# Kernel optimization log

Hardware: AMD Instinct MI355X
Metric: run time of the kernel (lower is better)

Reference implementation:

```python
import jax, jax.numpy as jnp
import numpy as np

K = 64        # num_clusters
S1 = 5        # num_shadow + 1
C = 128       # dim
ALPHA = 1500.0
EPS = 1e-12


def setup_inputs() -> dict:
    key = jax.random.key(0)
    k1, k2 = jax.random.split(key)
    x = jax.random.normal(k1, (8, C, 44, 44), dtype=jnp.float32)
    centroids = jax.random.normal(k2, (K, S1, C), dtype=jnp.float32) * 0.01
    return {"x": x, "centroids": centroids}


def reference(x, centroids):
    N = x.shape[0]
    # conv params derived from centroids, as in _init_params
    w = (2.0 * ALPHA) * centroids.reshape(K * S1, C)            # (K*S1, C)
    b = -ALPHA * jnp.linalg.norm(centroids.reshape(K * S1, C), axis=1)  # (K*S1,)

    xf = x.reshape(N, C, -1)                                    # (N, C, P)
    # 1x1 conv == GEMM over channel dim
    logits = jnp.einsum('mc,ncp->nmp', w, xf) + b[None, :, None]
    logits = logits.reshape(N, K, S1, -1)                       # (N, K, S1, P)

    soft_alpha = jax.nn.softmax(logits[:, :, 0:1, :], axis=1)   # (N, K, 1, P)
    soft_beta = jax.nn.softmax(logits, axis=2)[:, :, 0:1, :]    # (N, K, 1, P)
    soft_assign = soft_alpha * soft_beta                        # (N, K, 1, P)

    # residual = x - rep_centroid; then residual *= (1 + soft_assign); sum over P.
    # sum_p (x[n,c,p] - rep[k,c]) * w[n,k,p]
    #   = einsum(w, x) - rep[k,c] * sum_p w[n,k,p]   (same math, no (N,K,C,P) tensor)
    w_assign = 1.0 + soft_assign[:, :, 0, :]                    # (N, K, P)
    rep = centroids[:, 0, :]                                    # (K, C)
    out = jnp.einsum('nkp,ncp->nkc', w_assign, xf) \
          - rep[None, :, :] * jnp.sum(w_assign, axis=-1)[:, :, None]  # (N, K, C)

    # intra-cluster L2 normalize (dim=2), flatten, global L2 normalize
    out = out / jnp.maximum(jnp.linalg.norm(out, axis=2, keepdims=True), EPS)
    flat = out.reshape(N, -1)
    flat = flat / jnp.maximum(jnp.linalg.norm(flat, axis=1, keepdims=True), EPS)
    return (flat, soft_assign)
```

## Files before the change

### kernel.cpp

```cpp
#include <hip/hip_runtime.h>
#include <math.h>

#define NB 8
#define KC 64
#define S1C 5
#define CC 128
#define PP 1936
#define MM 320
#define PT 64
#define NPT 31
#define NTILE (NB * NPT)
#define ALPHAF 1500.0f
#define EPSF 1e-12f

#define WS_CENPK 65536
#define WS_GBIAS 512
#define WS_HDR   (WS_CENPK + WS_GBIAS)
#define WS_PART  ((size_t)NTILE * KC * CC)
#define WS_MAIN_FLOATS (WS_HDR + WS_PART + (size_t)NTILE * KC)

typedef __attribute__((ext_vector_type(8))) short short8;
typedef __attribute__((ext_vector_type(4))) float f32x4;

__device__ __forceinline__ unsigned pack_bf16s(float x) {
    unsigned u  = __float_as_uint(x);
    unsigned hi = u & 0xffff0000u;
    float lo    = x - __uint_as_float(hi);
    return hi | (__float_as_uint(lo) >> 16);
}

__device__ __forceinline__ void unpack8(const int4 q0, const int4 q1,
                                        short8& h, short8& l) {
    const int d[8] = {q0.x, q0.y, q0.z, q0.w, q1.x, q1.y, q1.z, q1.w};
#pragma unroll
    for (int j = 0; j < 8; ++j) {
        h[j] = (short)((unsigned)d[j] >> 16);
        l[j] = (short)((unsigned)d[j] & 0xffffu);
    }
}

__device__ __forceinline__ void split8(const float4 a, const float4 b,
                                       short8& h, short8& l) {
    const float f[8] = {a.x, a.y, a.z, a.w, b.x, b.y, b.z, b.w};
#pragma unroll
    for (int j = 0; j < 8; ++j) {
        const unsigned u  = __float_as_uint(f[j]);
        const unsigned hi = u & 0xffff0000u;
        const float lo    = f[j] - __uint_as_float(hi);
        h[j] = (short)(hi >> 16);
        l[j] = (short)(__float_as_uint(lo) >> 16);
    }
}

__global__ __launch_bounds__(64) void k0_pack(
    const float* __restrict__ cen, unsigned* __restrict__ cenPk,
    float* __restrict__ gbias)
{
    const int nt   = blockIdx.x;
    const int l    = threadIdx.x;
    const int l15  = l & 15;
    const int quad = l >> 4;
    const int mp   = nt * 16 + l15;
    const int s    = mp & 7;
    const bool valid = (s < 5);
    const int wrow = 5 * (mp >> 3) + s;
    short8* dst8 = (short8*)cenPk;
    float ss = 0.f;
#pragma unroll
    for (int ks = 0; ks < 4; ++ks) {
        float4 v0 = make_float4(0.f, 0.f, 0.f, 0.f), v1 = v0;
        if (valid) {
            const float* wp = cen + (size_t)wrow * CC + ks * 32 + quad * 8;
            v0 = *(const float4*)wp;
            v1 = *(const float4*)(wp + 4);
        }
        ss += v0.x * v0.x + v0.y * v0.y + v0.z * v0.z + v0.w * v0.w
            + v1.x * v1.x + v1.y * v1.y + v1.z * v1.z + v1.w * v1.w;
        short8 h, lo;
        split8(v0, v1, h, lo);
        const int base = ((ks * 32 + nt) * 64 + l) * 2;
        dst8[base]     = h;
        dst8[base + 1] = lo;
    }
    ss += __shfl_xor(ss, 16);
    ss += __shfl_xor(ss, 32);
    if (quad == 0) gbias[mp] = valid ? (-ALPHAF * sqrtf(ss)) : -3.0e38f;
}

__global__ __launch_bounds__(1024, 4) void k1_main(
    const float* __restrict__ x, const unsigned* __restrict__ cenPk,
    const float* __restrict__ gbias,
    float* __restrict__ sa_out, float* __restrict__ outC,
    float* __restrict__ outS, int mode)
{
    __shared__ unsigned xbuf[CC * 68];
    __shared__ unsigned war[KC * 68];
    __shared__ float2   ap[16 * 66];

    const int tid  = threadIdx.x;
    const int lane = tid & 63;
    const int wid  = tid >> 6;
    const int quad = lane >> 4;
    const int l15  = lane & 15;
    const int bx   = blockIdx.x;
    const int n    = bx / NPT;
    const int pt   = bx - n * NPT;
    const int p0   = pt * PT;

    float4 bvf[2];
#pragma unroll
    for (int i = 0; i < 2; ++i)
        bvf[i] = *(const float4*)(gbias + (2 * wid + i) * 16 + quad * 4);
    const short8* cpk8 = (const short8*)cenPk;
    short8 ch0[2], cl0[2];
#pragma unroll
    for (int i = 0; i < 2; ++i) {
        const int boff = ((2 * wid + i) * 64 + lane) * 2;
        ch0[i] = cpk8[boff];
        cl0[i] = cpk8[boff + 1];
    }

    const float* xn = x + (size_t)n * CC * PP;
    const int sc  = tid >> 3;
    const int spo = (tid & 7) * 8;
    unsigned pk[8];
    {
        float4 v0 = make_float4(0.f, 0.f, 0.f, 0.f), v1 = v0;
        if (p0 + spo < PP) {
            const float* src = xn + (size_t)sc * PP + p0 + spo;
            v0 = *(const float4*)src;
            v1 = *(const float4*)(src + 4);
        }
        pk[0] = pack_bf16s(v0.x); pk[1] = pack_bf16s(v0.y);
        pk[2] = pack_bf16s(v0.z); pk[3] = pack_bf16s(v0.w);
        pk[4] = pack_bf16s(v1.x); pk[5] = pack_bf16s(v1.y);
        pk[6] = pack_bf16s(v1.z); pk[7] = pack_bf16s(v1.w);
#pragma unroll
        for (int j = 0; j < 8; ++j) xbuf[(spo + j) * 132 + sc] = pk[j];
    }
    __syncthreads();

    f32x4 dacc[4][2];
#pragma unroll
    for (int a = 0; a < 4; ++a) {
        dacc[a][0] = (f32x4){0.f, 0.f, 0.f, 0.f};
        dacc[a][1] = (f32x4){0.f, 0.f, 0.f, 0.f};
    }

    auto mfma_step = [&](const int ksoff, const short8 ch[2], const short8 cl[2]) {
#pragma unroll
        for (int a = 0; a < 4; ++a) {
            const int abase = (a * 16 + l15) * 132 + ksoff + quad * 8;
            const int4 q0 = *(const int4*)(&xbuf[abase]);
            const int4 q1 = *(const int4*)(&xbuf[abase + 4]);
            short8 xh, xl;
            unpack8(q0, q1, xh, xl);
#pragma unroll
            for (int i = 0; i < 2; ++i) {
                dacc[a][i] = __builtin_amdgcn_mfma_f32_16x16x32_bf16(ch[i], xh, dacc[a][i], 0, 0, 0);
                dacc[a][i] = __builtin_amdgcn_mfma_f32_16x16x32_bf16(ch[i], xl, dacc[a][i], 0, 0, 0);
                dacc[a][i] = __builtin_amdgcn_mfma_f32_16x16x32_bf16(cl[i], xh, dacc[a][i], 0, 0, 0);
            }
        }
    };

    mfma_step(0, ch0, cl0);
#pragma unroll 1
    for (int ks = 1; ks < 4; ++ks) {
        short8 ch[2], cl[2];
#pragma unroll
        for (int i = 0; i < 2; ++i) {
            const int boff = ((ks * 32 + 2 * wid + i) * 64 + lane) * 2;
            ch[i] = cpk8[boff];
            cl[i] = cpk8[boff + 1];
        }
        mfma_step(ks * 32, ch, cl);
    }

#pragma unroll
    for (int i = 0; i < 2; ++i) {
        const float* bvp = (const float*)&bvf[i];
#pragma unroll
        for (int a = 0; a < 4; ++a)
#pragma unroll
            for (int r = 0; r < 4; ++r)
                dacc[a][i][r] = 2.f * ALPHAF * dacc[a][i][r] + bvp[r];
    }

#pragma unroll
    for (int a = 0; a < 4; ++a) {
        const float l0 = dacc[a][0][0];
        const float l1 = dacc[a][1][0];
        const float m2 = fmaxf(l0, l1);
        const float mo = __shfl_xor(m2, 32);
        const float m4 = fmaxf(m2, mo);
        float se = __expf(l0 - m4) + __expf(l1 - m4);
        se += __shfl_xor(se, 32);
        if ((lane & 48) == 0) ap[wid * 66 + a * 16 + l15] = make_float2(m4, se);
    }
    __syncthreads();

    *(int4*)(&xbuf[sc * 68 + spo])     = *(const int4*)&pk[0];
    *(int4*)(&xbuf[sc * 68 + spo + 4]) = *(const int4*)&pk[4];

    float gmv, arv;
    {
        float gm = -3.0e38f;
#pragma unroll
        for (int w = 0; w < 16; ++w) gm = fmaxf(gm, ap[w * 66 + lane].x);
        float s = 0.f;
#pragma unroll
        for (int w = 0; w < 16; ++w) {
            const float2 v = ap[w * 66 + lane];
            s += v.y * __expf(v.x - gm);
        }
        gmv = gm; arv = 1.0f / s;
    }

    const int  kb  = 4 * wid + ((lane >> 5) & 1);
    const bool evq = ((lane & 16) == 0);
    float psum2[2] = {0.f, 0.f};
#pragma unroll
    for (int a = 0; a < 4; ++a) {
        const int p = a * 16 + l15;
        const float gm_p = __shfl(gmv, p);
        const float ar_p = __shfl(arv, p);
        const bool pvalid = (p0 + p) < PP;
#pragma unroll
        for (int i = 0; i < 2; ++i) {
            const f32x4 lg = dacc[a][i];
            const float s4 = __shfl_xor(lg[0], 16);
            float m5 = fmaxf(fmaxf(lg[0], lg[1]), fmaxf(lg[2], lg[3]));
            m5 = fmaxf(m5, s4);
            const float e0 = __expf(lg[0] - m5);
            const float d5 = e0 + __expf(lg[1] - m5) + __expf(lg[2] - m5)
                           + __expf(lg[3] - m5) + __expf(s4 - m5);
            const float sa = __expf(lg[0] - gm_p) * ar_p * (e0 / d5);
            const float wa = pvalid ? (1.0f + sa) : 0.0f;
            if (evq) war[(kb + 2 * i) * 68 + p] = pack_bf16s(wa);
            psum2[i] += wa;
        }
    }
#pragma unroll
    for (int i = 0; i < 2; ++i) {
        float s = psum2[i];
        s += __shfl_xor(s, 1);
        s += __shfl_xor(s, 2);
        s += __shfl_xor(s, 4);
        s += __shfl_xor(s, 8);
        if ((lane & 31) == 0) {
            const int k = kb + 2 * i;
            if (mode == 0) outS[(size_t)bx * KC + k] = s;
            else           atomicAdd(&outS[(size_t)n * KC + k], s);
        }
    }
    __syncthreads();

    const int kt  = wid & 3;
    const int ct0 = (wid >> 2) * 2;
    f32x4 cacc[2];
    cacc[0] = (f32x4){0.f, 0.f, 0.f, 0.f};
    cacc[1] = (f32x4){0.f, 0.f, 0.f, 0.f};
#pragma unroll
    for (int ks = 0; ks < 64; ks += 32) {
        const int abase = (kt * 16 + l15) * 68 + ks + quad * 8;
        const int4 qa0 = *(const int4*)(&war[abase]);
        const int4 qa1 = *(const int4*)(&war[abase + 4]);
        short8 ah, al;
        unpack8(qa0, qa1, ah, al);
#pragma unroll
        for (int t = 0; t < 2; ++t) {
            const int c = (ct0 + t) * 16 + l15;
            const int bbase = c * 68 + ks + quad * 8;
            const int4 qb0 = *(const int4*)(&xbuf[bbase]);
            const int4 qb1 = *(const int4*)(&xbuf[bbase + 4]);
            short8 bh, bl;
            unpack8(qb0, qb1, bh, bl);
            cacc[t] = __builtin_amdgcn_mfma_f32_16x16x32_bf16(ah, bh, cacc[t], 0, 0, 0);
            cacc[t] = __builtin_amdgcn_mfma_f32_16x16x32_bf16(ah, bl, cacc[t], 0, 0, 0);
            cacc[t] = __builtin_amdgcn_mfma_f32_16x16x32_bf16(al, bh, cacc[t], 0, 0, 0);
        }
    }
    if (mode == 0) {
        float* dst = outC + (size_t)bx * KC * CC;
#pragma unroll
        for (int t = 0; t < 2; ++t) {
            const int c = (ct0 + t) * 16 + l15;
#pragma unroll
            for (int r = 0; r < 4; ++r)
                dst[(kt * 16 + 4 * quad + r) * CC + c] = cacc[t][r];
        }
    } else {
        float* dst = outC + (size_t)n * KC * CC;
#pragma unroll
        for (int t = 0; t < 2; ++t) {
            const int c = (ct0 + t) * 16 + l15;
#pragma unroll
            for (int r = 0; r < 4; ++r)
                atomicAdd(&dst[(kt * 16 + 4 * quad + r) * CC + c], cacc[t][r]);
        }
    }

    {
        float* san = sa_out + (size_t)n * KC * PP;
        const int k  = tid >> 4;
        const int p4 = (tid & 15) * 4;
        const int pg = p0 + p4;
        if (pg < PP) {
            const int4 q = *(const int4*)(&war[k * 68 + p4]);
            const int d[4] = {q.x, q.y, q.z, q.w};
            float4 sv;
            float* svp = &sv.x;
#pragma unroll
            for (int j = 0; j < 4; ++j) {
                const unsigned u = (unsigned)d[j];
                const float wa = __uint_as_float(u & 0xffff0000u)
                               + __uint_as_float(u << 16);
                svp[j] = wa - 1.0f;
            }
            *(float4*)(&san[(size_t)k * PP + pg]) = sv;
        }
    }
}

__global__ __launch_bounds__(128) void k2_slab(
    const float* __restrict__ part, const float* __restrict__ ps,
    const float* __restrict__ cen, float* __restrict__ flat)
{
    __shared__ float w2[2];
    const int b = blockIdx.x;
    const int n = b >> 6;
    const int k = b & 63;
    const int c = threadIdx.x;
    const float* pb = part + (size_t)n * NPT * KC * CC + (size_t)k * CC + c;
    float v = 0.f;
#pragma unroll 8
    for (int pt = 0; pt < NPT; ++pt) v += pb[(size_t)pt * KC * CC];
    const float* psb = ps + (size_t)n * NPT * KC + k;
    float sw = 0.f;
#pragma unroll
    for (int pt = 0; pt < NPT; ++pt) sw += psb[(size_t)pt * KC];
    v -= cen[(size_t)k * S1C * CC + c] * sw;

    float ss = v * v;
#pragma unroll
    for (int off = 32; off > 0; off >>= 1) ss += __shfl_down(ss, off);
    if ((c & 63) == 0) w2[c >> 6] = ss;
    __syncthreads();
    const float norm = sqrtf(w2[0] + w2[1]);
    const float scale = 1.0f / (fmaxf(norm, EPSF) * 8.0f);
    flat[(size_t)b * CC + c] = v * scale;
}

__global__ __launch_bounds__(128) void k2_final(
    const float* __restrict__ accC, const float* __restrict__ accS,
    const float* __restrict__ cen, float* __restrict__ flat)
{
    __shared__ float w2[2];
    const int b = blockIdx.x;
    const int k = b & 63;
    const int c = threadIdx.x;
    const float v = accC[(size_t)b * CC + c] -
                    cen[(size_t)k * S1C * CC + c] * accS[b];
    float ss = v * v;
#pragma unroll
    for (int off = 32; off > 0; off >>= 1) ss += __shfl_down(ss, off);
    if ((c & 63) == 0) w2[c >> 6] = ss;
    __syncthreads();
    const float norm = sqrtf(w2[0] + w2[1]);
    const float scale = 1.0f / (fmaxf(norm, EPSF) * 8.0f);
    flat[(size_t)b * CC + c] = v * scale;
}

extern "C" void kernel_launch(void* const* d_in, const int* in_sizes, int n_in,
                              void* d_out, int out_size, void* d_ws, size_t ws_size,
                              hipStream_t stream) {
    const float* x   = (const float*)d_in[0];
    const float* cen = (const float*)d_in[1];
    float* out  = (float*)d_out;
    float* flat = out;
    float* sa   = out + (size_t)NB * KC * CC;
    float* ws   = (float*)d_ws;

    unsigned* cenPk = (unsigned*)ws;
    float*    gbias = ws + WS_CENPK;

    if (ws_size >= WS_MAIN_FLOATS * 4) {
        float* part = ws + WS_HDR;
        float* ps   = part + WS_PART;
        k0_pack<<<32, 64, 0, stream>>>(cen, cenPk, gbias);
        k1_main<<<NTILE, 1024, 0, stream>>>(x, cenPk, gbias, sa, part, ps, 0);
        k2_slab<<<NB * KC, 128, 0, stream>>>(part, ps, cen, flat);
    } else {
        float* accC = ws + WS_HDR;
        float* accS = accC + (size_t)NB * KC * CC;
        hipMemsetAsync(accC, 0, (size_t)(NB * KC * CC + NB * KC) * 4, stream);
        k0_pack<<<32, 64, 0, stream>>>(cen, cenPk, gbias);
        k1_main<<<NTILE, 1024, 0, stream>>>(x, cenPk, gbias, sa, accC, accS, 1);
        k2_final<<<NB * KC, 128, 0, stream>>>(accC, accS, cen, flat);
    }
}
```

Before: 80.62 us.

## Store split bf16 hi/lo planes in XOR-swizzled LDS instead of packed words

Replaces the packed hi|lo 32-bit LDS buffers with separate bf16 high and low planes for x (in both p-major and c-major layouts) and for the assignment weights, all using XOR swizzling. MFMA operands now load directly as short8 vectors with no unpack shuffles. The global x load switches to per-channel strided scalar loads along p. The change also removes the second LDS rewrite of x after the first GEMM. It raises static LDS use (about 80KB versus about 60KB), which may reduce occupancy. It also adds 16-bit scalar scattered stores into the transposed buffers.

Result: no change. 81.56 us (+1.2%).

```diff
diff --git a/kernel.cpp b/kernel.cpp
--- a/kernel.cpp
+++ b/kernel.cpp
@@ -21,23 +21,6 @@
 
 typedef __attribute__((ext_vector_type(8))) short short8;
 typedef __attribute__((ext_vector_type(4))) float f32x4;
-
-__device__ __forceinline__ unsigned pack_bf16s(float x) {
-    unsigned u  = __float_as_uint(x);
-    unsigned hi = u & 0xffff0000u;
-    float lo    = x - __uint_as_float(hi);
-    return hi | (__float_as_uint(lo) >> 16);
-}
-
-__device__ __forceinline__ void unpack8(const int4 q0, const int4 q1,
-                                        short8& h, short8& l) {
-    const int d[8] = {q0.x, q0.y, q0.z, q0.w, q1.x, q1.y, q1.z, q1.w};
-#pragma unroll
-    for (int j = 0; j < 8; ++j) {
-        h[j] = (short)((unsigned)d[j] >> 16);
-        l[j] = (short)((unsigned)d[j] & 0xffffu);
-    }
-}
 
 __device__ __forceinline__ void split8(const float4 a, const float4 b,
                                        short8& h, short8& l) {
@@ -93,9 +76,13 @@
     float* __restrict__ sa_out, float* __restrict__ outC,
     float* __restrict__ outS, int mode)
 {
-    __shared__ unsigned xbuf[CC * 68];
-    __shared__ unsigned war[KC * 68];
-    __shared__ float2   ap[16 * 66];
+    __shared__ __align__(16) unsigned short xh [64 * 128];
+    __shared__ __align__(16) unsigned short xl [64 * 128];
+    __shared__ __align__(16) unsigned short xch[128 * 64];
+    __shared__ __align__(16) unsigned short xcl[128 * 64];
+    __shared__ __align__(16) unsigned short wah[64 * 64];
+    __shared__ __align__(16) unsigned short wal[64 * 64];
+    __shared__ float2 ap[16 * 66];
 
     const int tid  = threadIdx.x;
     const int lane = tid & 63;
@@ -121,22 +108,36 @@
     }
 
     const float* xn = x + (size_t)n * CC * PP;
-    const int sc  = tid >> 3;
-    const int spo = (tid & 7) * 8;
-    unsigned pk[8];
     {
-        float4 v0 = make_float4(0.f, 0.f, 0.f, 0.f), v1 = v0;
-        if (p0 + spo < PP) {
-            const float* src = xn + (size_t)sc * PP + p0 + spo;
-            v0 = *(const float4*)src;
-            v1 = *(const float4*)(src + 4);
-        }
-        pk[0] = pack_bf16s(v0.x); pk[1] = pack_bf16s(v0.y);
-        pk[2] = pack_bf16s(v0.z); pk[3] = pack_bf16s(v0.w);
-        pk[4] = pack_bf16s(v1.x); pk[5] = pack_bf16s(v1.y);
-        pk[6] = pack_bf16s(v1.z); pk[7] = pack_bf16s(v1.w);
-#pragma unroll
-        for (int j = 0; j < 8; ++j) xbuf[(spo + j) * 132 + sc] = pk[j];
+        const int pl = tid & 63;
+        const int c0 = (tid >> 6) * 8;
+        const bool pv = (p0 + pl) < PP;
+        const float* src = xn + p0 + pl;
+        float v[8];
+#pragma unroll
+        for (int i = 0; i < 8; ++i)
+            v[i] = pv ? src[(size_t)(c0 + i) * PP] : 0.f;
+        unsigned short hv[8], lv[8];
+#pragma unroll
+        for (int i = 0; i < 8; ++i) {
+            const unsigned u  = __float_as_uint(v[i]);
+            const unsigned hi = u & 0xffff0000u;
+            hv[i] = (unsigned short)(hi >> 16);
+            lv[i] = (unsigned short)(__float_as_uint(v[i] - __uint_as_float(hi)) >> 16);
+        }
+        short8 H8, L8;
+#pragma unroll
+        for (int i = 0; i < 8; ++i) { H8[i] = (short)hv[i]; L8[i] = (short)lv[i]; }
+        const int sx = (pl * 128 + c0) ^ ((pl & 7) << 3);
+        *(short8*)&xh[sx] = H8;
+        *(short8*)&xl[sx] = L8;
+#pragma unroll
+        for (int i = 0; i < 8; ++i) {
+            const int ci  = c0 + i;
+            const int sc2 = (ci * 64 + pl) ^ ((ci & 7) << 3);
+            xch[sc2] = hv[i];
+            xcl[sc2] = lv[i];
+        }
     }
     __syncthreads();
 
@@ -150,16 +151,15 @@
     auto mfma_step = [&](const int ksoff, const short8 ch[2], const short8 cl[2]) {
 #pragma unroll
         for (int a = 0; a < 4; ++a) {
-            const int abase = (a * 16 + l15) * 132 + ksoff + quad * 8;
-            const int4 q0 = *(const int4*)(&xbuf[abase]);
-            const int4 q1 = *(const int4*)(&xbuf[abase + 4]);
-            short8 xh, xl;
-            unpack8(q0, q1, xh, xl);
+            const int arow = a * 16 + l15;
+            const int sidx = (arow * 128 + ksoff + quad * 8) ^ ((arow & 7) << 3);
+            const short8 xh8 = *(const short8*)&xh[sidx];
+            const short8 xl8 = *(const short8*)&xl[sidx];
 #pragma unroll
             for (int i = 0; i < 2; ++i) {
-                dacc[a][i] = __builtin_amdgcn_mfma_f32_16x16x32_bf16(ch[i], xh, dacc[a][i], 0, 0, 0);
-                dacc[a][i] = __builtin_amdgcn_mfma_f32_16x16x32_bf16(ch[i], xl, dacc[a][i], 0, 0, 0);
-                dacc[a][i] = __builtin_amdgcn_mfma_f32_16x16x32_bf16(cl[i], xh, dacc[a][i], 0, 0, 0);
+                dacc[a][i] = __builtin_amdgcn_mfma_f32_16x16x32_bf16(ch[i], xh8, dacc[a][i], 0, 0, 0);
+                dacc[a][i] = __builtin_amdgcn_mfma_f32_16x16x32_bf16(ch[i], xl8, dacc[a][i], 0, 0, 0);
+                dacc[a][i] = __builtin_amdgcn_mfma_f32_16x16x32_bf16(cl[i], xh8, dacc[a][i], 0, 0, 0);
             }
         }
     };
@@ -199,9 +199,6 @@
         if ((lane & 48) == 0) ap[wid * 66 + a * 16 + l15] = make_float2(m4, se);
     }
     __syncthreads();
-
-    *(int4*)(&xbuf[sc * 68 + spo])     = *(const int4*)&pk[0];
-    *(int4*)(&xbuf[sc * 68 + spo + 4]) = *(const int4*)&pk[4];
 
     float gmv, arv;
     {
@@ -237,7 +234,14 @@
                            + __expf(lg[3] - m5) + __expf(s4 - m5);
             const float sa = __expf(lg[0] - gm_p) * ar_p * (e0 / d5);
             const float wa = pvalid ? (1.0f + sa) : 0.0f;
-            if (evq) war[(kb + 2 * i) * 68 + p] = pack_bf16s(wa);
+            if (evq) {
+                const int kk = kb + 2 * i;
+                const int si = (kk * 64 + p) ^ ((kk & 7) << 3);
+                const unsigned u  = __float_as_uint(wa);
+                const unsigned hi = u & 0xffff0000u;
+                wah[si] = (unsigned short)(hi >> 16);
+                wal[si] = (unsigned short)(__float_as_uint(wa - __uint_as_float(hi)) >> 16);
+            }
             psum2[i] += wa;
         }
     }
@@ -263,19 +267,16 @@
     cacc[1] = (f32x4){0.f, 0.f, 0.f, 0.f};
 #pragma unroll
     for (int ks = 0; ks < 64; ks += 32) {
-        const int abase = (kt * 16 + l15) * 68 + ks + quad * 8;
-        const int4 qa0 = *(const int4*)(&war[abase]);
-        const int4 qa1 = *(const int4*)(&war[abase + 4]);
-        short8 ah, al;
-        unpack8(qa0, qa1, ah, al);
+        const int arow = kt * 16 + l15;
+        const int sa_  = (arow * 64 + ks + quad * 8) ^ ((arow & 7) << 3);
+        const short8 ah = *(const short8*)&wah[sa_];
+        const short8 al = *(const short8*)&wal[sa_];
 #pragma unroll
         for (int t = 0; t < 2; ++t) {
-            const int c = (ct0 + t) * 16 + l15;
-            const int bbase = c * 68 + ks + quad * 8;
-            const int4 qb0 = *(const int4*)(&xbuf[bbase]);
-            const int4 qb1 = *(const int4*)(&xbuf[bbase + 4]);
-            short8 bh, bl;
-            unpack8(qb0, qb1, bh, bl);
+            const int crow = (ct0 + t) * 16 + l15;
+            const int sb   = (crow * 64 + ks + quad * 8) ^ ((crow & 7) << 3);
+            const short8 bh = *(const short8*)&xch[sb];
+            const short8 bl = *(const short8*)&xcl[sb];
             cacc[t] = __builtin_amdgcn_mfma_f32_16x16x32_bf16(ah, bh, cacc[t], 0, 0, 0);
             cacc[t] = __builtin_amdgcn_mfma_f32_16x16x32_bf16(ah, bl, cacc[t], 0, 0, 0);
             cacc[t] = __builtin_amdgcn_mfma_f32_16x16x32_bf16(al, bh, cacc[t], 0, 0, 0);
@@ -307,18 +308,20 @@
         const int p4 = (tid & 15) * 4;
         const int pg = p0 + p4;
         if (pg < PP) {
-            const int4 q = *(const int4*)(&war[k * 68 + p4]);
-            const int d[4] = {q.x, q.y, q.z, q.w};
-            float4 sv;
-            float* svp = &sv.x;
+            const int si = (k * 64 + p4) ^ ((k & 7) << 3);
+            const uint2 qh = *(const uint2*)&wah[si];
+            const uint2 ql = *(const uint2*)&wal[si];
+            const unsigned hh[2] = {qh.x, qh.y};
+            const unsigned ll[2] = {ql.x, ql.y};
+            float4 sv; float* svp = &sv.x;
 #pragma unroll
             for (int j = 0; j < 4; ++j) {
-                const unsigned u = (unsigned)d[j];
-                const float wa = __uint_as_float(u & 0xffff0000u)
-                               + __uint_as_float(u << 16);
+                const unsigned h16 = (hh[j >> 1] >> ((j & 1) * 16)) & 0xffffu;
+                const unsigned l16 = (ll[j >> 1] >> ((j & 1) * 16)) & 0xffffu;
+                const float wa = __uint_as_float(h16 << 16) + __uint_as_float(l16 << 16);
                 svp[j] = wa - 1.0f;
             }
-            *(float4*)(&san[(size_t)k * PP + pg]) = sv;
+            *(float4*)&san[(size_t)k * PP + pg] = sv;
         }
     }
 }
```
